# Optimization experiments

Measured on AMD Instinct MI355X. Metric: run time of the kernel, lower is better.

## Reference

```python
import jax, jax.numpy as jnp
import numpy as np

DIM = 256
HEADS = 8
WS = 8          # window_size[0]
N = WS * WS     # tokens per window
B = 2048        # number of windows (batch * windows_per_image)


def _rel_pos_indices(ws):
    # Reproduces: grid of (i,j) positions flattened, pairwise diff, shifted, flattened index
    pos = np.arange(ws)
    gy, gx = np.meshgrid(pos, pos, indexing='ij')
    grid = np.stack([gy.ravel(), gx.ravel()], axis=-1)          # (ws*ws, 2)
    rel = grid[:, None, :] - grid[None, :, :] + (ws - 1)        # (n, n, 2)
    idx = rel[..., 0] * (2 * ws - 1) + rel[..., 1]              # (n, n)
    return jnp.asarray(idx, dtype=jnp.int32)


def setup_inputs() -> dict:
    key = jax.random.key(0)
    ks = jax.random.split(key, 6)
    return {
        'x': jax.random.normal(ks[0], (B, N, DIM), dtype=jnp.float32),
        'qkv_w': jax.random.normal(ks[1], (3 * DIM, DIM), dtype=jnp.float32) * 0.02,
        'qkv_b': jax.random.normal(ks[2], (3 * DIM,), dtype=jnp.float32) * 0.02,
        'proj_w': jax.random.normal(ks[3], (DIM, DIM), dtype=jnp.float32) * 0.02,
        'proj_b': jax.random.normal(ks[4], (DIM,), dtype=jnp.float32) * 0.02,
        'bias_table': jax.random.normal(ks[5], ((2 * WS - 1) ** 2, HEADS), dtype=jnp.float32) * 0.02,
        'rel_pos_indices': _rel_pos_indices(WS),
    }


def reference(x, qkv_w, qkv_b, proj_w, proj_b, bias_table, rel_pos_indices):
    b, n, c = x.shape
    head_dim = c // HEADS
    scale = head_dim ** (-0.5)

    qkv = x @ qkv_w.T + qkv_b                                   # [b, n, 3c]
    q, k, v = jnp.split(qkv, 3, axis=-1)
    # b n (h d) -> b h n d
    to_heads = lambda t: t.reshape(b, n, HEADS, head_dim).transpose(0, 2, 1, 3)
    q, k, v = to_heads(q) * scale, to_heads(k), to_heads(v)

    # relative position bias: [n, n, h] -> [h, n, n]
    bias = bias_table[rel_pos_indices].transpose(2, 0, 1)

    attn = jnp.einsum('bhnd,bhmd->bhnm', q, k) + bias           # [b, h, n, n]
    attn = jax.nn.softmax(attn, axis=-1)
    out = jnp.einsum('bhnm,bhmd->bhnd', attn, v)                # [b, h, n, d]
    out = out.transpose(0, 2, 1, 3).reshape(b, n, c)
    out = out @ proj_w.T + proj_b
    return (out, attn)
```

## Files before the change

### kernel.cpp

```cpp
#include <hip/hip_runtime.h>

typedef __bf16 bf16;
typedef __attribute__((ext_vector_type(8))) __bf16 bf16x8;
typedef __attribute__((ext_vector_type(4))) __bf16 bf16x4;
typedef __attribute__((ext_vector_type(4))) float f32x4;

#define MFMA16(A, Bf, Cf) __builtin_amdgcn_mfma_f32_16x16x32_bf16((A), (Bf), (Cf), 0, 0, 0)

namespace {
constexpr int kB = 2048;
constexpr int kN = 64;
constexpr int kC = 256;
constexpr int kH = 8;
constexpr float kScale = 0.17677669529663687f;
constexpr size_t kOut0 = (size_t)kB * kN * kC;
constexpr size_t kWqkvOff = 0;
constexpr size_t kWprojOff = 393216;
constexpr size_t kBiasOff = 524288;
}

__global__ void prep_kernel(const float* __restrict__ qkv_w,
                            const float* __restrict__ proj_w,
                            const float* __restrict__ bias_table,
                            const int* __restrict__ rel_idx,
                            bf16* __restrict__ qkv_wb,
                            bf16* __restrict__ proj_wb,
                            float* __restrict__ biasf) {
  int t = blockIdx.x * 256 + threadIdx.x;
  if (t < 196608) {
    qkv_wb[t] = (bf16)qkv_w[t];
  } else if (t < 262144) {
    int u = t - 196608;
    proj_wb[u] = (bf16)proj_w[u];
  } else if (t < 294912) {
    int u = t - 262144;
    int h = u >> 12;
    int v = u & 4095;
    int wv = v >> 10;
    int ct = (v >> 8) & 3;
    int lane = (v >> 2) & 63;
    int r = v & 3;
    int row = wv * 16 + (lane >> 4) * 4 + r;
    int col = ct * 16 + (lane & 15);
    biasf[u] = bias_table[rel_idx[row * 64 + col] * 8 + h];
  }
}

__launch_bounds__(256, 2)
__global__ void attn_kernel(const float* __restrict__ x,
                            const float* __restrict__ qkv_b,
                            const float* __restrict__ proj_b,
                            const bf16* __restrict__ qkv_wb,
                            const bf16* __restrict__ proj_wb,
                            const float* __restrict__ biasf,
                            float* __restrict__ out,
                            float* __restrict__ attn_out) {
  __shared__ __align__(16) bf16 xb[64 * 264];
  __shared__ __align__(16) bf16 qkbuf[2 * 2 * 64 * 40];
  __shared__ __align__(16) bf16 vTb[2 * 32 * 72];
  __shared__ __align__(16) bf16 Pb[64 * 72];
  __shared__ __align__(16) bf16 ohs[4 * 16 * 40];

  const int t = threadIdx.x;
  const int wave = t >> 6;
  const int lane = t & 63;
  const int l16 = lane & 15;
  const int quad = lane >> 4;
  const int b = blockIdx.x;
  const int mrow = wave * 16 + l16;

  const f32x4 fzero = {0.f, 0.f, 0.f, 0.f};

  {
    const f32x4* xv = (const f32x4*)(x + (size_t)b * (kN * kC));
#pragma unroll
    for (int i = 0; i < 16; ++i) {
      int g4 = i * 256 + t;
      f32x4 v = xv[g4];
      int row = g4 >> 6;
      int c4 = (g4 & 63) << 2;
      bf16x4 w;
      w.x = (bf16)v.x; w.y = (bf16)v.y; w.z = (bf16)v.z; w.w = (bf16)v.w;
      *(bf16x4*)&xb[row * 264 + c4] = w;
    }
  }
  __syncthreads();

  f32x4 pacc[16];
#pragma unroll
  for (int i = 0; i < 16; ++i) pacc[i] = fzero;

  for (int h = 0; h < kH; ++h) {
    const int buf = h & 1;
    bf16* qh = qkbuf + buf * (2 * 64 * 40);
    bf16* kh = qh + 64 * 40;
    bf16* vT = vTb + buf * (32 * 72);

    f32x4 bfrag[4];
    const f32x4* bp4 = (const f32x4*)(biasf + h * 4096 + wave * 1024);
#pragma unroll
    for (int ct = 0; ct < 4; ++ct) bfrag[ct] = bp4[ct * 64 + lane];
    float qbv[6];
#pragma unroll
    for (int nt = 0; nt < 6; ++nt) {
      int col = (nt & 1) * 16 + l16;
      qbv[nt] = qkv_b[((nt < 2) ? 0 : (nt < 4) ? 256 : 512) + h * 32 + col];
    }

    bf16x8 afr[8];
#pragma unroll
    for (int kt = 0; kt < 8; ++kt)
      afr[kt] = *(const bf16x8*)&xb[mrow * 264 + kt * 32 + quad * 8];

    f32x4 acc[6];
#pragma unroll
    for (int nt = 0; nt < 6; ++nt) acc[nt] = fzero;
#pragma unroll
    for (int nt = 0; nt < 6; ++nt) {
      int wrow = (nt < 2) ? (h * 32 + nt * 16 + l16)
               : (nt < 4) ? (256 + h * 32 + (nt - 2) * 16 + l16)
                          : (512 + h * 32 + (nt - 4) * 16 + l16);
      const bf16* wp = qkv_wb + wrow * 256 + quad * 8;
      bf16x8 bfr[8];
#pragma unroll
      for (int kt = 0; kt < 8; ++kt) bfr[kt] = *(const bf16x8*)&wp[kt * 32];
#pragma unroll
      for (int kt = 0; kt < 8; ++kt) acc[nt] = MFMA16(afr[kt], bfr[kt], acc[nt]);
    }

#pragma unroll
    for (int nt = 0; nt < 6; ++nt) {
      float qb = qbv[nt];
#pragma unroll
      for (int r = 0; r < 4; ++r) {
        int row = wave * 16 + quad * 4 + r;
        int col = (nt & 1) * 16 + l16;
        float val = acc[nt][r] + qb;
        if (nt < 2)       qh[row * 40 + col] = (bf16)(val * kScale);
        else if (nt < 4)  kh[row * 40 + col] = (bf16)val;
        else              vT[col * 72 + row] = (bf16)val;
      }
    }
    __syncthreads();

    bf16x8 aS = *(const bf16x8*)&qh[mrow * 40 + quad * 8];
    f32x4 s[4];
#pragma unroll
    for (int ct = 0; ct < 4; ++ct) {
      bf16x8 bS = *(const bf16x8*)&kh[(ct * 16 + l16) * 40 + quad * 8];
      s[ct] = MFMA16(aS, bS, bfrag[ct]);
    }

#pragma unroll
    for (int r = 0; r < 4; ++r) {
      float m = fmaxf(fmaxf(s[0][r], s[1][r]), fmaxf(s[2][r], s[3][r]));
#pragma unroll
      for (int off = 8; off; off >>= 1) m = fmaxf(m, __shfl_xor(m, off));
      float e0 = __expf(s[0][r] - m);
      float e1 = __expf(s[1][r] - m);
      float e2 = __expf(s[2][r] - m);
      float e3 = __expf(s[3][r] - m);
      float sum = (e0 + e1) + (e2 + e3);
#pragma unroll
      for (int off = 8; off; off >>= 1) sum += __shfl_xor(sum, off);
      float is = 1.0f / sum;
      s[0][r] = e0 * is; s[1][r] = e1 * is; s[2][r] = e2 * is; s[3][r] = e3 * is;
    }

    float* ao = attn_out + ((size_t)(b * kH + h) << 12);
#pragma unroll
    for (int ct = 0; ct < 4; ++ct)
#pragma unroll
      for (int r = 0; r < 4; ++r) {
        int i = wave * 16 + quad * 4 + r;
        int j = ct * 16 + l16;
        float pv = s[ct][r];
        ao[i * 64 + j] = pv;
        Pb[i * 72 + j] = (bf16)pv;
      }

    f32x4 o[2];
    o[0] = fzero; o[1] = fzero;
#pragma unroll
    for (int ks = 0; ks < 2; ++ks) {
      bf16x8 aP = *(const bf16x8*)&Pb[mrow * 72 + ks * 32 + quad * 8];
#pragma unroll
      for (int nt = 0; nt < 2; ++nt) {
        bf16x8 bV = *(const bf16x8*)&vT[(nt * 16 + l16) * 72 + ks * 32 + quad * 8];
        o[nt] = MFMA16(aP, bV, o[nt]);
      }
    }

    bf16* oh = ohs + wave * (16 * 40);
#pragma unroll
    for (int nt = 0; nt < 2; ++nt)
#pragma unroll
      for (int r = 0; r < 4; ++r)
        oh[(quad * 4 + r) * 40 + nt * 16 + l16] = (bf16)o[nt][r];

    bf16x8 aO = *(const bf16x8*)&oh[l16 * 40 + quad * 8];
#pragma unroll
    for (int nt = 0; nt < 16; ++nt) {
      bf16x8 bW = *(const bf16x8*)&proj_wb[(nt * 16 + l16) * 256 + h * 32 + quad * 8];
      pacc[nt] = MFMA16(aO, bW, pacc[nt]);
    }
  }

  float* op = out + (size_t)b * (kN * kC);
#pragma unroll
  for (int nt = 0; nt < 16; ++nt) {
    float pb = proj_b[nt * 16 + l16];
#pragma unroll
    for (int r = 0; r < 4; ++r) {
      int i = wave * 16 + quad * 4 + r;
      op[i * 256 + nt * 16 + l16] = pacc[nt][r] + pb;
    }
  }
}

extern "C" void kernel_launch(void* const* d_in, const int* in_sizes, int n_in,
                              void* d_out, int out_size, void* d_ws, size_t ws_size,
                              hipStream_t stream) {
  const float* x          = (const float*)d_in[0];
  const float* qkv_w      = (const float*)d_in[1];
  const float* qkv_b      = (const float*)d_in[2];
  const float* proj_w     = (const float*)d_in[3];
  const float* proj_b     = (const float*)d_in[4];
  const float* bias_table = (const float*)d_in[5];
  const int*   rel_idx    = (const int*)d_in[6];

  bf16*  qkv_wb = (bf16*)((char*)d_ws + kWqkvOff);
  bf16*  proj_wb = (bf16*)((char*)d_ws + kWprojOff);
  float* biasf  = (float*)((char*)d_ws + kBiasOff);

  float* out      = (float*)d_out;
  float* attn_out = out + kOut0;

  prep_kernel<<<1152, 256, 0, stream>>>(qkv_w, proj_w, bias_table, rel_idx,
                                        qkv_wb, proj_wb, biasf);
  attn_kernel<<<kB, 256, 0, stream>>>(x, qkv_b, proj_b, qkv_wb, proj_wb, biasf,
                                      out, attn_out);
}
```

Baseline: 891.8 us.

## Alias x staging with per-head LDS buffers and keep x fragments in registers

The x fragments each wave needs are loaded from LDS once, before the head loop, and kept in registers instead of being re-read for every head. Because x is no longer read from LDS after that point, its staging buffer is put in a union with the per-head buffers for Q, K, V, P and the output tile. Q now has a single buffer, which is safe because each wave only reads its own rows. The smaller LDS footprint allows launch bounds of three blocks per CU instead of two, aiming to hide latency better. The trade-off is more register pressure from the persistent fragments under a tighter register budget, which risks spills.

After: 965.2 us. 1.08x slower.

```diff
diff --git a/kernel.cpp b/kernel.cpp
--- a/kernel.cpp
+++ b/kernel.cpp
@@ -46,7 +46,7 @@
   }
 }
 
-__launch_bounds__(256, 2)
+__launch_bounds__(256, 3)
 __global__ void attn_kernel(const float* __restrict__ x,
                             const float* __restrict__ qkv_b,
                             const float* __restrict__ proj_b,
@@ -55,11 +55,17 @@
                             const float* __restrict__ biasf,
                             float* __restrict__ out,
                             float* __restrict__ attn_out) {
-  __shared__ __align__(16) bf16 xb[64 * 264];
-  __shared__ __align__(16) bf16 qkbuf[2 * 2 * 64 * 40];
-  __shared__ __align__(16) bf16 vTb[2 * 32 * 72];
-  __shared__ __align__(16) bf16 Pb[64 * 72];
-  __shared__ __align__(16) bf16 ohs[4 * 16 * 40];
+  union SMemU {
+    bf16 xb[64 * 264];
+    struct {
+      bf16 qh[64 * 40];
+      bf16 kh[2][64 * 40];
+      bf16 vT[2][32 * 72];
+      bf16 Pb[64 * 72];
+      bf16 ohs[4][16 * 40];
+    } lp;
+  };
+  __shared__ __align__(16) SMemU sm;
 
   const int t = threadIdx.x;
   const int wave = t >> 6;
@@ -81,9 +87,15 @@
       int c4 = (g4 & 63) << 2;
       bf16x4 w;
       w.x = (bf16)v.x; w.y = (bf16)v.y; w.z = (bf16)v.z; w.w = (bf16)v.w;
-      *(bf16x4*)&xb[row * 264 + c4] = w;
-    }
-  }
+      *(bf16x4*)&sm.xb[row * 264 + c4] = w;
+    }
+  }
+  __syncthreads();
+
+  bf16x8 afr[8];
+#pragma unroll
+  for (int kt = 0; kt < 8; ++kt)
+    afr[kt] = *(const bf16x8*)&sm.xb[mrow * 264 + kt * 32 + quad * 8];
   __syncthreads();
 
   f32x4 pacc[16];
@@ -92,9 +104,9 @@
 
   for (int h = 0; h < kH; ++h) {
     const int buf = h & 1;
-    bf16* qh = qkbuf + buf * (2 * 64 * 40);
-    bf16* kh = qh + 64 * 40;
-    bf16* vT = vTb + buf * (32 * 72);
+    bf16* qh = sm.lp.qh;
+    bf16* kh = sm.lp.kh[buf];
+    bf16* vT = sm.lp.vT[buf];
 
     f32x4 bfrag[4];
     const f32x4* bp4 = (const f32x4*)(biasf + h * 4096 + wave * 1024);
@@ -106,11 +118,6 @@
       int col = (nt & 1) * 16 + l16;
       qbv[nt] = qkv_b[((nt < 2) ? 0 : (nt < 4) ? 256 : 512) + h * 32 + col];
     }
-
-    bf16x8 afr[8];
-#pragma unroll
-    for (int kt = 0; kt < 8; ++kt)
-      afr[kt] = *(const bf16x8*)&xb[mrow * 264 + kt * 32 + quad * 8];
 
     f32x4 acc[6];
 #pragma unroll
@@ -176,14 +183,14 @@
         int j = ct * 16 + l16;
         float pv = s[ct][r];
         ao[i * 64 + j] = pv;
-        Pb[i * 72 + j] = (bf16)pv;
+        sm.lp.Pb[i * 72 + j] = (bf16)pv;
       }
 
     f32x4 o[2];
     o[0] = fzero; o[1] = fzero;
 #pragma unroll
     for (int ks = 0; ks < 2; ++ks) {
-      bf16x8 aP = *(const bf16x8*)&Pb[mrow * 72 + ks * 32 + quad * 8];
+      bf16x8 aP = *(const bf16x8*)&sm.lp.Pb[mrow * 72 + ks * 32 + quad * 8];
 #pragma unroll
       for (int nt = 0; nt < 2; ++nt) {
         bf16x8 bV = *(const bf16x8*)&vT[(nt * 16 + l16) * 72 + ks * 32 + quad * 8];
@@ -191,7 +198,7 @@
       }
     }
 
-    bf16* oh = ohs + wave * (16 * 40);
+    bf16* oh = sm.lp.ohs[wave];
 #pragma unroll
     for (int nt = 0; nt < 2; ++nt)
 #pragma unroll
```

## Defer output projection, reuse x LDS buffer for head outputs, raise occupancy

Applied to the files above, without the earlier changes.

Each wave now loads its x A-fragments into registers once before the head loop instead of on every head. Per-head attention outputs are written back into the x shared buffer, and the output projection runs as one K=256 GEMM after the loop, so the 16 projection accumulators no longer stay live across the loop. Shared memory is cut by dropping double buffering and aliasing the P buffer with the q buffer, and launch bounds rise to 3 blocks per CU. In exchange, an extra barrier per head is needed to protect the single-buffered q/k/v, and the lower register budget risks spills.

New measurement: 898.0 us. About the same (+0.7%).

```diff
diff --git a/kernel.cpp b/kernel.cpp
--- a/kernel.cpp
+++ b/kernel.cpp
@@ -46,7 +46,7 @@
   }
 }
 
-__launch_bounds__(256, 2)
+__launch_bounds__(256, 3)
 __global__ void attn_kernel(const float* __restrict__ x,
                             const float* __restrict__ qkv_b,
                             const float* __restrict__ proj_b,
@@ -55,11 +55,10 @@
                             const float* __restrict__ biasf,
                             float* __restrict__ out,
                             float* __restrict__ attn_out) {
-  __shared__ __align__(16) bf16 xb[64 * 264];
-  __shared__ __align__(16) bf16 qkbuf[2 * 2 * 64 * 40];
-  __shared__ __align__(16) bf16 vTb[2 * 32 * 72];
-  __shared__ __align__(16) bf16 Pb[64 * 72];
-  __shared__ __align__(16) bf16 ohs[4 * 16 * 40];
+  __shared__ __align__(16) bf16 xo[64 * 264];
+  __shared__ __align__(16) bf16 qp[64 * 72];
+  __shared__ __align__(16) bf16 kh[64 * 40];
+  __shared__ __align__(16) bf16 vT[32 * 72];
 
   const int t = threadIdx.x;
   const int wave = t >> 6;
@@ -81,21 +80,17 @@
       int c4 = (g4 & 63) << 2;
       bf16x4 w;
       w.x = (bf16)v.x; w.y = (bf16)v.y; w.z = (bf16)v.z; w.w = (bf16)v.w;
-      *(bf16x4*)&xb[row * 264 + c4] = w;
+      *(bf16x4*)&xo[row * 264 + c4] = w;
     }
   }
   __syncthreads();
 
-  f32x4 pacc[16];
-#pragma unroll
-  for (int i = 0; i < 16; ++i) pacc[i] = fzero;
+  bf16x8 afr[8];
+#pragma unroll
+  for (int kt = 0; kt < 8; ++kt)
+    afr[kt] = *(const bf16x8*)&xo[mrow * 264 + kt * 32 + quad * 8];
 
   for (int h = 0; h < kH; ++h) {
-    const int buf = h & 1;
-    bf16* qh = qkbuf + buf * (2 * 64 * 40);
-    bf16* kh = qh + 64 * 40;
-    bf16* vT = vTb + buf * (32 * 72);
-
     f32x4 bfrag[4];
     const f32x4* bp4 = (const f32x4*)(biasf + h * 4096 + wave * 1024);
 #pragma unroll
@@ -106,11 +101,6 @@
       int col = (nt & 1) * 16 + l16;
       qbv[nt] = qkv_b[((nt < 2) ? 0 : (nt < 4) ? 256 : 512) + h * 32 + col];
     }
-
-    bf16x8 afr[8];
-#pragma unroll
-    for (int kt = 0; kt < 8; ++kt)
-      afr[kt] = *(const bf16x8*)&xb[mrow * 264 + kt * 32 + quad * 8];
 
     f32x4 acc[6];
 #pragma unroll
@@ -128,6 +118,8 @@
       for (int kt = 0; kt < 8; ++kt) acc[nt] = MFMA16(afr[kt], bfr[kt], acc[nt]);
     }
 
+    __syncthreads();
+
 #pragma unroll
     for (int nt = 0; nt < 6; ++nt) {
       float qb = qbv[nt];
@@ -136,14 +128,14 @@
         int row = wave * 16 + quad * 4 + r;
         int col = (nt & 1) * 16 + l16;
         float val = acc[nt][r] + qb;
-        if (nt < 2)       qh[row * 40 + col] = (bf16)(val * kScale);
+        if (nt < 2)       qp[row * 72 + col] = (bf16)(val * kScale);
         else if (nt < 4)  kh[row * 40 + col] = (bf16)val;
         else              vT[col * 72 + row] = (bf16)val;
       }
     }
     __syncthreads();
 
-    bf16x8 aS = *(const bf16x8*)&qh[mrow * 40 + quad * 8];
+    bf16x8 aS = *(const bf16x8*)&qp[mrow * 72 + quad * 8];
     f32x4 s[4];
 #pragma unroll
     for (int ct = 0; ct < 4; ++ct) {
@@ -176,14 +168,14 @@
         int j = ct * 16 + l16;
         float pv = s[ct][r];
         ao[i * 64 + j] = pv;
-        Pb[i * 72 + j] = (bf16)pv;
+        qp[i * 72 + j] = (bf16)pv;
       }
 
     f32x4 o[2];
     o[0] = fzero; o[1] = fzero;
 #pragma unroll
     for (int ks = 0; ks < 2; ++ks) {
-      bf16x8 aP = *(const bf16x8*)&Pb[mrow * 72 + ks * 32 + quad * 8];
+      bf16x8 aP = *(const bf16x8*)&qp[mrow * 72 + ks * 32 + quad * 8];
 #pragma unroll
       for (int nt = 0; nt < 2; ++nt) {
         bf16x8 bV = *(const bf16x8*)&vT[(nt * 16 + l16) * 72 + ks * 32 + quad * 8];
@@ -191,19 +183,30 @@
       }
     }
 
-    bf16* oh = ohs + wave * (16 * 40);
 #pragma unroll
     for (int nt = 0; nt < 2; ++nt)
 #pragma unroll
       for (int r = 0; r < 4; ++r)
-        oh[(quad * 4 + r) * 40 + nt * 16 + l16] = (bf16)o[nt][r];
-
-    bf16x8 aO = *(const bf16x8*)&oh[l16 * 40 + quad * 8];
-#pragma unroll
-    for (int nt = 0; nt < 16; ++nt) {
-      bf16x8 bW = *(const bf16x8*)&proj_wb[(nt * 16 + l16) * 256 + h * 32 + quad * 8];
-      pacc[nt] = MFMA16(aO, bW, pacc[nt]);
-    }
+        xo[(wave * 16 + quad * 4 + r) * 264 + h * 32 + nt * 16 + l16] =
+            (bf16)o[nt][r];
+  }
+
+  bf16x8 oafr[8];
+#pragma unroll
+  for (int kt = 0; kt < 8; ++kt)
+    oafr[kt] = *(const bf16x8*)&xo[mrow * 264 + kt * 32 + quad * 8];
+
+  f32x4 pacc[16];
+#pragma unroll
+  for (int i = 0; i < 16; ++i) pacc[i] = fzero;
+#pragma unroll
+  for (int nt = 0; nt < 16; ++nt) {
+    const bf16* wp = proj_wb + (nt * 16 + l16) * 256 + quad * 8;
+    bf16x8 bfr[8];
+#pragma unroll
+    for (int kt = 0; kt < 8; ++kt) bfr[kt] = *(const bf16x8*)&wp[kt * 32];
+#pragma unroll
+    for (int kt = 0; kt < 8; ++kt) pacc[nt] = MFMA16(oafr[kt], bfr[kt], pacc[nt]);
   }
 
   float* op = out + (size_t)b * (kN * kC);
```
